# Kernel tuning notes

Hardware: AMD Instinct MI355X
Metric: run time of the kernel (lower is better)

## Reference

```python
import jax, jax.numpy as jnp
import numpy as np
from jax import lax

EPS = 1e-6  # LayerNorm2d eps


def _ln2d(x, w, b):
    # channel-wise LayerNorm over dim 1 of [B,C,H,W]
    mu = jnp.mean(x, axis=1, keepdims=True)
    var = jnp.mean((x - mu) ** 2, axis=1, keepdims=True)
    return (x - mu) / jnp.sqrt(var + EPS) * w[None, :, None, None] + b[None, :, None, None]


def _conv1x1(x, w, b):
    # w: [O, C]
    return jnp.einsum('bchw,oc->bohw', x, w) + b[None, :, None, None]


def _dconv(x, w, b):
    # 3x3 conv, dilation 4, padding 4 -> same H,W. w: [O, C, 3, 3]
    y = lax.conv_general_dilated(x, w, window_strides=(1, 1),
                                 padding=((4, 4), (4, 4)), rhs_dilation=(4, 4),
                                 dimension_numbers=('NCHW', 'OIHW', 'NCHW'))
    return y + b[None, :, None, None]


def _forward(x_l, x_r, nl_w, nl_b, nr_w, nr_b, lp1_w, lp1_b, rp1_w, rp1_b,
             dl_w, dl_b, dr_w, dr_b, lp2_w, lp2_b, rp2_w, rp2_b, beta, gamma):
    c = x_l.shape[1]
    scale = c ** (-0.5)
    N_l = _ln2d(x_l, nl_w, nl_b)
    N_r = _ln2d(x_r, nr_w, nr_b)
    V_l = jnp.transpose(_conv1x1(x_l, lp2_w, lp2_b), (0, 2, 3, 1))   # [B,H,W,C]
    V_r = jnp.transpose(_conv1x1(x_r, rp2_w, rp2_b), (0, 2, 3, 1))
    Q_l = jnp.transpose(_conv1x1(N_l, lp1_w, lp1_b), (0, 2, 3, 1))   # [B,H,W,C]
    Q_r = jnp.transpose(_conv1x1(N_r, rp1_w, rp1_b), (0, 2, 3, 1))
    K_l_T = jnp.transpose(_dconv(N_l, dl_w, dl_b), (0, 2, 1, 3))     # [B,H,C,W]
    K_r_T = jnp.transpose(_dconv(N_r, dr_w, dr_b), (0, 2, 1, 3))
    # per-row cross attention: [B,H,W,W]
    attn_r2l = jnp.einsum('bhwc,bhcv->bhwv', Q_l, K_r_T) * scale
    attn_l2r = jnp.einsum('bhwc,bhcv->bhwv', Q_r, K_l_T) * scale
    F_r2l = jnp.einsum('bhwv,bhvc->bhwc', jax.nn.softmax(attn_r2l, axis=-1), V_r)
    F_l2r = jnp.einsum('bhwv,bhvc->bhwc', jax.nn.softmax(attn_l2r, axis=-1), V_l)
    F_r2l = jnp.transpose(F_r2l, (0, 3, 1, 2)) * beta   # [B,C,H,W]
    F_l2r = jnp.transpose(F_l2r, (0, 3, 1, 2)) * gamma
    return x_l + F_r2l, x_r + F_l2r


def setup_inputs() -> dict:
    key = jax.random.key(0)
    ks = jax.random.split(key, 12)
    B, C, H, W = 2, 128, 192, 512
    s = 0.02
    rn = lambda k, shp: s * jax.random.normal(k, shp, jnp.float32)
    return {
        'x_l': jax.random.normal(ks[0], (B, C, H, W), jnp.float32),
        'x_r': jax.random.normal(ks[1], (B, C, H, W), jnp.float32),
        'nl_w': jnp.ones((C,), jnp.float32), 'nl_b': jnp.zeros((C,), jnp.float32),
        'nr_w': jnp.ones((C,), jnp.float32), 'nr_b': jnp.zeros((C,), jnp.float32),
        'lp1_w': rn(ks[2], (C, C)), 'lp1_b': jnp.zeros((C,), jnp.float32),
        'rp1_w': rn(ks[3], (C, C)), 'rp1_b': jnp.zeros((C,), jnp.float32),
        'dl_w': rn(ks[4], (C, C, 3, 3)), 'dl_b': jnp.zeros((C,), jnp.float32),
        'dr_w': rn(ks[5], (C, C, 3, 3)), 'dr_b': jnp.zeros((C,), jnp.float32),
        'lp2_w': rn(ks[6], (C, C)), 'lp2_b': jnp.zeros((C,), jnp.float32),
        'rp2_w': rn(ks[7], (C, C)), 'rp2_b': jnp.zeros((C,), jnp.float32),
        'beta': 0.1 * jax.random.normal(ks[8], (1, C, 1, 1), jnp.float32),
        'gamma': 0.1 * jax.random.normal(ks[9], (1, C, 1, 1), jnp.float32),
    }


def reference(x_l, x_r, nl_w, nl_b, nr_w, nr_b, lp1_w, lp1_b, rp1_w, rp1_b,
              dl_w, dl_b, dr_w, dr_b, lp2_w, lp2_b, rp2_w, rp2_b, beta, gamma):
    return _forward(x_l, x_r, nl_w, nl_b, nr_w, nr_b, lp1_w, lp1_b, rp1_w, rp1_b,
                    dl_w, dl_b, dr_w, dr_b, lp2_w, lp2_b, rp2_w, rp2_b, beta, gamma)
```

## Files before the change

kernel.cpp:

```cpp
#include <hip/hip_runtime.h>
#include <stdint.h>

#define CC 128
#define HH 192
#define WW 512
#define BB 2
#define HW (HH*WW)
#define CHW (CC*HW)
#define TENS (BB*CHW)

typedef __attribute__((ext_vector_type(8))) short bf16x8;
typedef __attribute__((ext_vector_type(4))) short bf16x4;
typedef __attribute__((ext_vector_type(4))) float f32x4;

__device__ __forceinline__ unsigned short f2bf(float f) {
    union { float f; unsigned u; } v; v.f = f;
    return (unsigned short)((v.u + 0x7FFFu + ((v.u >> 16) & 1u)) >> 16);
}
__device__ __forceinline__ float bf2f(unsigned short u) {
    union { unsigned u; float f; } v; v.u = ((unsigned)u) << 16;
    return v.f;
}
__device__ __forceinline__ uint32_t cvtpk(float lo, float hi) {
    uint32_t r;
    asm("v_cvt_pk_bf16_f32 %0, %1, %2" : "=v"(r) : "v"(lo), "v"(hi));
    return r;
}
__device__ __forceinline__ f32x4 MFMA(bf16x8 a, bf16x8 b, f32x4 c) {
    return __builtin_amdgcn_mfma_f32_16x16x32_bf16(a, b, c, 0, 0, 0);
}
__device__ __forceinline__ f32x4 MFMA16(bf16x4 a, bf16x4 b, f32x4 c) {
#if __has_builtin(__builtin_amdgcn_mfma_f32_16x16x16_bf16)
    return __builtin_amdgcn_mfma_f32_16x16x16_bf16(a, b, c, 0, 0, 0);
#elif __has_builtin(__builtin_amdgcn_mfma_f32_16x16x16bf16_1k)
    return __builtin_amdgcn_mfma_f32_16x16x16bf16_1k(a, b, c, 0, 0, 0);
#else
    f32x4 d = c;
    asm("v_mfma_f32_16x16x16_bf16 %0, %1, %2, %0" : "+v"(d) : "v"(a), "v"(b));
    return d;
#endif
}

__global__ __launch_bounds__(256) void wcast_k(
    const float* __restrict__ dlw, const float* __restrict__ drw,
    unsigned short* __restrict__ wd)
{
    int i = blockIdx.x * 256 + threadIdx.x;
    if (i >= 2 * 9 * CC * CC) return;
    int e  = i & 7;
    int l  = (i >> 3) & 63;
    int n_ = (i >> 9) & 3;
    int kk = (i >> 11) & 3;
    int oh = (i >> 13) & 1;
    int rest = i >> 14;
    int tap = rest % 9;
    int side = rest / 9;
    int o = oh * 64 + n_ * 16 + (l & 15);
    int c = kk * 32 + (l >> 4) * 8 + e;
    const float* src = side ? drw : dlw;
    wd[i] = f2bf(src[((size_t)o * CC + c) * 9 + tap]);
}

__global__ __launch_bounds__(256) void lnv_k(
    const float* __restrict__ xl, const float* __restrict__ xr,
    const float* __restrict__ nlw, const float* __restrict__ nlb,
    const float* __restrict__ nrw, const float* __restrict__ nrb,
    const float* __restrict__ wlp, const float* __restrict__ blp,
    const float* __restrict__ wrp, const float* __restrict__ brp,
    unsigned short* __restrict__ ntl, unsigned short* __restrict__ ntr,
    unsigned short* __restrict__ vlo, unsigned short* __restrict__ vro)
{
    const int side = blockIdx.y;
    const float* x  = side ? xr : xl;
    const float* nw = side ? nrw : nlw;
    const float* nb = side ? nrb : nlb;
    const float* wv = side ? wrp : wlp;
    const float* bv = side ? brp : blp;
    unsigned short* nt = side ? ntr : ntl;
    unsigned short* vo = side ? vro : vlo;
    const int bid = blockIdx.x;
    const int wt = bid & 7, h = (bid >> 3) % HH, b = bid / (8 * HH);
    const int w0 = wt * 64;
    const int t = threadIdx.x;

    __shared__ unsigned short sA[64][136];
    __shared__ unsigned short sB[128][136];
    __shared__ float red[8][64];
    __shared__ float smu[64], srs[64];

    {
        const int w = t & 63, cg = t >> 6;
        const float* xp = x + (size_t)b * CHW + (size_t)h * WW + w0 + w;
        float s = 0.f, q = 0.f;
        for (int i = 0; i < 16; i++) {
            int c = cg * 32 + i * 2;
            float v0 = xp[(size_t)c * HW];
            float v1 = xp[(size_t)(c + 1) * HW];
            *(uint32_t*)&sA[w][c] = cvtpk(v0, v1);
            s += v0 + v1; q += v0 * v0 + v1 * v1;
        }
        red[cg][w] = s; red[4 + cg][w] = q;
    }
    for (int it = 0; it < 16; it++) {
        int f = it * 1024 + t * 4;
        int o = f >> 7, c = f & 127;
        float4 v = *(const float4*)(wv + o * CC + c);
        *(uint32_t*)&sB[o][c]     = cvtpk(v.x, v.y);
        *(uint32_t*)&sB[o][c + 2] = cvtpk(v.z, v.w);
    }
    __syncthreads();
    if (t < 64) {
        float S = red[0][t] + red[1][t] + red[2][t] + red[3][t];
        float Q = red[4][t] + red[5][t] + red[6][t] + red[7][t];
        float mu = S * (1.f / CC);
        float var = fmaxf(Q * (1.f / CC) - mu * mu, 0.f);
        smu[t] = mu; srs[t] = rsqrtf(var + 1e-6f);
    }
    __syncthreads();
    {
        const int cl = (t & 63) * 2, wg = t >> 6;
        const float nwa = nw[cl], nwb = nw[cl + 1];
        const float nba = nb[cl], nbb = nb[cl + 1];
        unsigned short* npb = nt + ((size_t)(b * HH + h) * WW + w0) * CC;
        for (int wp = 0; wp < 16; wp++) {
            int w = wp * 4 + wg;
            float mu = smu[w], rs = srs[w];
            float v0 = (bf2f(sA[w][cl]) - mu) * rs * nwa + nba;
            float v1 = (bf2f(sA[w][cl + 1]) - mu) * rs * nwb + nbb;
            *(uint32_t*)&npb[(size_t)w * CC + cl] = cvtpk(v0, v1);
        }
    }
    const int wid = t >> 6, l = t & 63, lr = l & 15, lg = l >> 4;
    f32x4 acc[8] = {};
    for (int kk = 0; kk < 4; kk++) {
        bf16x8 a = *(const bf16x8*)&sA[wid * 16 + lr][kk * 32 + lg * 8];
#pragma unroll
        for (int n_ = 0; n_ < 8; n_++) {
            bf16x8 bb = *(const bf16x8*)&sB[n_ * 16 + lr][kk * 32 + lg * 8];
            acc[n_] = MFMA(a, bb, acc[n_]);
        }
    }
    unsigned short* vp = vo + ((size_t)(b * HH + h) * CC) * WW + w0;
    for (int n_ = 0; n_ < 8; n_++) {
        int o = n_ * 16 + lr;
        float bias = bv[o];
        uint2 uu;
        uu.x = cvtpk(acc[n_][0] + bias, acc[n_][1] + bias);
        uu.y = cvtpk(acc[n_][2] + bias, acc[n_][3] + bias);
        *(uint2*)&vp[(size_t)o * WW + wid * 16 + lg * 4] = uu;
    }
}

__global__ __launch_bounds__(256) void dconv_k(
    const unsigned short* __restrict__ ntl, const unsigned short* __restrict__ ntr,
    const unsigned short* __restrict__ wfr,
    const float* __restrict__ dlb, const float* __restrict__ drb,
    unsigned short* __restrict__ klo, unsigned short* __restrict__ kro)
{
    const int side = blockIdx.y;
    const unsigned short* nt = side ? ntr : ntl;
    const unsigned short* wbase = wfr + (size_t)side * 9 * 16384;
    const float* bd = side ? drb : dlb;
    unsigned short* ko = side ? kro : klo;
    const int bid0 = blockIdx.x;
    const int lgc = (bid0 & 7) * 192 + (bid0 >> 3);
    const int wt = lgc & 3;
    const int hb = lgc >> 2;
    const int h = hb % HH, b = hb / HH;
    const int w0 = wt * 128;
    const int t = threadIdx.x;
    const int wid = t >> 6, l = t & 63, lr = l & 15, lg = l >> 4;
    const int whalf = wid & 1, ohalf = wid >> 1;

    __shared__ unsigned short sA[136][136];

    f32x4 acc[4][4] = {};
    for (int dy = 0; dy < 3; dy++) {
        const int hh = h + 4 * (dy - 1);
        const bool hok = (hh >= 0 && hh < HH);
        __syncthreads();
        for (int f = t * 8; f < 136 * 128; f += 2048) {
            int wloc = f >> 7, c = f & 127;
            int w = w0 - 4 + wloc;
            bf16x8 v = {0, 0, 0, 0, 0, 0, 0, 0};
            if (hok && w >= 0 && w < WW)
                v = *(const bf16x8*)(nt + ((size_t)(b * HH + hh) * WW + w) * CC + c);
            *(bf16x8*)&sA[wloc][c] = v;
        }
        __syncthreads();
#pragma unroll
        for (int dx = 0; dx < 3; dx++) {
            const unsigned short* wtap =
                wbase + (size_t)(dy * 3 + dx) * 16384 + ohalf * 8192 + l * 8;
#pragma unroll
            for (int kk = 0; kk < 4; kk++) {
                bf16x8 bfr[4];
#pragma unroll
                for (int n_ = 0; n_ < 4; n_++)
                    bfr[n_] = *(const bf16x8*)(wtap + (kk * 4 + n_) * 512);
                bf16x8 af[4];
#pragma unroll
                for (int g = 0; g < 4; g++)
                    af[g] = *(const bf16x8*)&sA[whalf * 64 + g * 16 + lr + 4 * dx][kk * 32 + lg * 8];
#pragma unroll
                for (int g = 0; g < 4; g++)
#pragma unroll
                    for (int n_ = 0; n_ < 4; n_++)
                        acc[g][n_] = MFMA(af[g], bfr[n_], acc[g][n_]);
            }
        }
    }
    unsigned short* kp = ko + ((size_t)(b * HH + h) * WW + w0) * CC;
    for (int g = 0; g < 4; g++)
        for (int n_ = 0; n_ < 4; n_++) {
            int o = ohalf * 64 + n_ * 16 + lr;
            float bias = bd[o];
            for (int j = 0; j < 4; j++) {
                int w = whalf * 64 + g * 16 + lg * 4 + j;
                kp[(size_t)w * CC + o] = f2bf(acc[g][n_][j] + bias);
            }
        }
}

__global__ __launch_bounds__(256, 2) void attn_k(
    const unsigned short* __restrict__ ntl, const unsigned short* __restrict__ ntr,
    const unsigned short* __restrict__ kl,  const unsigned short* __restrict__ kr,
    const unsigned short* __restrict__ vtl, const unsigned short* __restrict__ vtr,
    const float* __restrict__ lp1w, const float* __restrict__ lp1b,
    const float* __restrict__ rp1w, const float* __restrict__ rp1b,
    const float* __restrict__ xl, const float* __restrict__ xr,
    const float* __restrict__ beta, const float* __restrict__ gamma,
    float* __restrict__ out)
{
    __shared__ __align__(16) char smem[52224];
    unsigned short* sQ  = (unsigned short*)smem;
    unsigned short* sWh = (unsigned short*)(smem + 34816);
    unsigned short* sKt = (unsigned short*)smem;
    unsigned short* sVt = (unsigned short*)(smem + 17408);

    const int dir = blockIdx.z;
    const unsigned short* nq  = dir ? ntr : ntl;
    const unsigned short* kws = dir ? kl : kr;
    const unsigned short* vws = dir ? vtl : vtr;
    const float* wq   = dir ? rp1w : lp1w;
    const float* bq   = dir ? rp1b : lp1b;
    const float* xres = dir ? xr : xl;
    const float* mult = dir ? gamma : beta;
    float* op = out + (size_t)dir * TENS;

    const int bid = blockIdx.x;
    const int xcd = bid & 7;
    const int s   = bid >> 3;
    const int qb  = s & 3;
    const int bh  = xcd + 8 * (s >> 2);
    const int q0  = qb * 128;
    const int t = threadIdx.x;
    const int wid = t >> 6, l = t & 63, lr = l & 15, lg = l >> 4;

    const unsigned short* ksrc = kws + (size_t)bh * WW * CC;
    const unsigned short* vsrc = vws + (size_t)bh * CC * WW;

    bf16x8 kreg[4], vreg[4];
#pragma unroll
    for (int it = 0; it < 4; it++) {
        int f = it * 2048 + t * 8;
        kreg[it] = *(const bf16x8*)(ksrc + f);
    }
#pragma unroll
    for (int it = 0; it < 4; it++) {
        int f = it * 2048 + t * 8;
        int c = f >> 6, k = f & 63;
        vreg[it] = *(const bf16x8*)(vsrc + (size_t)c * WW + k);
    }

    {
        const unsigned short* nsrc = nq + ((size_t)bh * WW + q0) * CC;
        for (int it = 0; it < 8; it++) {
            int f = it * 2048 + t * 8;
            *(bf16x8*)&sQ[(f >> 7) * 136 + (f & 127)] = *(const bf16x8*)(nsrc + f);
        }
        for (int it = 0; it < 8; it++) {
            int f = it * 1024 + t * 4;
            int o = f >> 7, c = f & 127;
            float4 v = *(const float4*)(wq + o * CC + c);
            *(uint32_t*)&sWh[o * 136 + c]     = cvtpk(v.x, v.y);
            *(uint32_t*)&sWh[o * 136 + c + 2] = cvtpk(v.z, v.w);
        }
    }
    f32x4 qacc[2][8] = {};
    __syncthreads();
    for (int kk = 0; kk < 4; kk++) {
        bf16x8 a0 = *(const bf16x8*)&sQ[(wid * 32 + lr) * 136 + kk * 32 + lg * 8];
        bf16x8 a1 = *(const bf16x8*)&sQ[(wid * 32 + 16 + lr) * 136 + kk * 32 + lg * 8];
#pragma unroll
        for (int n_ = 0; n_ < 4; n_++) {
            bf16x8 b = *(const bf16x8*)&sWh[(n_ * 16 + lr) * 136 + kk * 32 + lg * 8];
            qacc[0][n_] = MFMA(a0, b, qacc[0][n_]);
            qacc[1][n_] = MFMA(a1, b, qacc[1][n_]);
        }
    }
    __syncthreads();
    for (int it = 0; it < 8; it++) {
        int f = it * 1024 + t * 4;
        int o = f >> 7, c = f & 127;
        float4 v = *(const float4*)(wq + (o + 64) * CC + c);
        *(uint32_t*)&sWh[o * 136 + c]     = cvtpk(v.x, v.y);
        *(uint32_t*)&sWh[o * 136 + c + 2] = cvtpk(v.z, v.w);
    }
    __syncthreads();
    for (int kk = 0; kk < 4; kk++) {
        bf16x8 a0 = *(const bf16x8*)&sQ[(wid * 32 + lr) * 136 + kk * 32 + lg * 8];
        bf16x8 a1 = *(const bf16x8*)&sQ[(wid * 32 + 16 + lr) * 136 + kk * 32 + lg * 8];
#pragma unroll
        for (int n_ = 0; n_ < 4; n_++) {
            bf16x8 b = *(const bf16x8*)&sWh[(n_ * 16 + lr) * 136 + kk * 32 + lg * 8];
            qacc[0][4 + n_] = MFMA(a0, b, qacc[0][4 + n_]);
            qacc[1][4 + n_] = MFMA(a1, b, qacc[1][4 + n_]);
        }
    }
    __syncthreads();
    {
        const float SCL = 0.08838834764831845f * 1.4426950408889634f;
#pragma unroll
        for (int mg = 0; mg < 2; mg++)
#pragma unroll
            for (int n_ = 0; n_ < 8; n_++) {
                float bias = bq[n_ * 16 + lr];
#pragma unroll
                for (int j = 0; j < 4; j++)
                    sQ[(wid * 32 + mg * 16 + lg * 4 + j) * 136 + n_ * 16 + lr] =
                        f2bf((qacc[mg][n_][j] + bias) * SCL);
            }
    }
    __syncthreads();
    bf16x8 qf[2][4];
#pragma unroll
    for (int qg = 0; qg < 2; qg++)
#pragma unroll
        for (int kk = 0; kk < 4; kk++)
            qf[qg][kk] = *(const bf16x8*)&sQ[(wid * 32 + qg * 16 + lr) * 136 + kk * 32 + lg * 8];

    f32x4 oacc[8][2] = {};
    float mrow[2] = {-1e30f, -1e30f};
    float lrow[2] = {0.f, 0.f};

    for (int kb = 0; kb < 8; kb++) {
        __syncthreads();
#pragma unroll
        for (int it = 0; it < 4; it++) {
            int f = it * 2048 + t * 8;
            *(bf16x8*)&sKt[(f >> 7) * 136 + (f & 127)] = kreg[it];
        }
#pragma unroll
        for (int it = 0; it < 4; it++) {
            int f = it * 2048 + t * 8;
            int c = f >> 6, k = f & 63;
            *(bf16x8*)&sVt[c * 72 + k] = vreg[it];
        }
        if (kb < 7) {
#pragma unroll
            for (int it = 0; it < 4; it++) {
                int f = it * 2048 + t * 8;
                kreg[it] = *(const bf16x8*)(ksrc + (kb + 1) * 64 * CC + f);
            }
#pragma unroll
            for (int it = 0; it < 4; it++) {
                int f = it * 2048 + t * 8;
                int c = f >> 6, k = f & 63;
                vreg[it] = *(const bf16x8*)(vsrc + (size_t)c * WW + (kb + 1) * 64 + k);
            }
        }
        __syncthreads();
        f32x4 sacc[2][4] = {};
        __builtin_amdgcn_s_setprio(1);
        for (int kk = 0; kk < 4; kk++)
#pragma unroll
            for (int n_ = 0; n_ < 4; n_++) {
                bf16x8 kf = *(const bf16x8*)&sKt[(n_ * 16 + lr) * 136 + kk * 32 + lg * 8];
                sacc[0][n_] = MFMA(kf, qf[0][kk], sacc[0][n_]);
                sacc[1][n_] = MFMA(kf, qf[1][kk], sacc[1][n_]);
            }
        __builtin_amdgcn_s_setprio(0);
        float pm[2];
#pragma unroll
        for (int qg = 0; qg < 2; qg++) {
            float m_ = sacc[qg][0][0];
#pragma unroll
            for (int n_ = 0; n_ < 4; n_++)
#pragma unroll
                for (int j = 0; j < 4; j++) m_ = fmaxf(m_, sacc[qg][n_][j]);
            m_ = fmaxf(m_, __shfl_xor(m_, 16, 64));
            m_ = fmaxf(m_, __shfl_xor(m_, 32, 64));
            pm[qg] = m_;
        }
        bool need = (pm[0] - mrow[0] > 8.f) || (pm[1] - mrow[1] > 8.f);
        if (__any(need)) {
            float al[2];
#pragma unroll
            for (int qg = 0; qg < 2; qg++) {
                float mn = fmaxf(mrow[qg], pm[qg]);
                al[qg] = exp2f(mrow[qg] - mn);
                mrow[qg] = mn;
                lrow[qg] *= al[qg];
            }
#pragma unroll
            for (int n_ = 0; n_ < 8; n_++)
#pragma unroll
                for (int qg = 0; qg < 2; qg++) {
                    f32x4 o = oacc[n_][qg];
                    o[0] *= al[qg]; o[1] *= al[qg]; o[2] *= al[qg]; o[3] *= al[qg];
                    oacc[n_][qg] = o;
                }
        }
#pragma unroll
        for (int qg = 0; qg < 2; qg++) {
            float rs = 0.f;
#pragma unroll
            for (int n_ = 0; n_ < 4; n_++)
#pragma unroll
                for (int j = 0; j < 4; j++) {
                    float e = exp2f(sacc[qg][n_][j] - mrow[qg]);
                    sacc[qg][n_][j] = e;
                    rs += e;
                }
            rs += __shfl_xor(rs, 16, 64);
            rs += __shfl_xor(rs, 32, 64);
            lrow[qg] += rs;
        }
        __builtin_amdgcn_s_setprio(1);
#pragma unroll
        for (int n_ = 0; n_ < 4; n_++) {
            union { uint32_t u[2]; bf16x4 v; } b0, b1;
            b0.u[0] = cvtpk(sacc[0][n_][0], sacc[0][n_][1]);
            b0.u[1] = cvtpk(sacc[0][n_][2], sacc[0][n_][3]);
            b1.u[0] = cvtpk(sacc[1][n_][0], sacc[1][n_][1]);
            b1.u[1] = cvtpk(sacc[1][n_][2], sacc[1][n_][3]);
#pragma unroll
            for (int n8 = 0; n8 < 8; n8++) {
                bf16x4 va = *(const bf16x4*)&sVt[(n8 * 16 + lr) * 72 + n_ * 16 + lg * 4];
                oacc[n8][0] = MFMA16(va, b0.v, oacc[n8][0]);
                oacc[n8][1] = MFMA16(va, b1.v, oacc[n8][1]);
            }
        }
        __builtin_amdgcn_s_setprio(0);
    }

    const float inv0 = 1.f / lrow[0], inv1 = 1.f / lrow[1];
    const int b = bh / HH, h = bh % HH;
    const int w_0 = q0 + wid * 32 + lr;
    const float* xp0 = xres + (size_t)b * CHW + (size_t)h * WW + w_0;
    float* outp0 = op + (size_t)b * CHW + (size_t)h * WW + w_0;
#pragma unroll
    for (int n_ = 0; n_ < 8; n_++) {
        float4 m4 = *(const float4*)&mult[n_ * 16 + lg * 4];
#pragma unroll
        for (int j = 0; j < 4; j++) {
            int c = n_ * 16 + lg * 4 + j;
            float mj = (&m4.x)[j];
            outp0[(size_t)c * HW]      = xp0[(size_t)c * HW]      + oacc[n_][0][j] * inv0 * mj;
            outp0[(size_t)c * HW + 16] = xp0[(size_t)c * HW + 16] + oacc[n_][1][j] * inv1 * mj;
        }
    }
}

extern "C" void kernel_launch(void* const* d_in, const int* in_sizes, int n_in,
                              void* d_out, int out_size, void* d_ws, size_t ws_size,
                              hipStream_t stream)
{
    const float* xl   = (const float*)d_in[0];
    const float* xr   = (const float*)d_in[1];
    const float* nlw  = (const float*)d_in[2];
    const float* nlb  = (const float*)d_in[3];
    const float* nrw  = (const float*)d_in[4];
    const float* nrb  = (const float*)d_in[5];
    const float* lp1w = (const float*)d_in[6];
    const float* lp1b = (const float*)d_in[7];
    const float* rp1w = (const float*)d_in[8];
    const float* rp1b = (const float*)d_in[9];
    const float* dlw  = (const float*)d_in[10];
    const float* dlb  = (const float*)d_in[11];
    const float* drw  = (const float*)d_in[12];
    const float* drb  = (const float*)d_in[13];
    const float* lp2w = (const float*)d_in[14];
    const float* lp2b = (const float*)d_in[15];
    const float* rp2w = (const float*)d_in[16];
    const float* rp2b = (const float*)d_in[17];
    const float* beta = (const float*)d_in[18];
    const float* gamma= (const float*)d_in[19];
    float* out = (float*)d_out;

    unsigned short* ws = (unsigned short*)d_ws;
    const size_t A = (size_t)TENS;
    unsigned short* Ntl = ws;
    unsigned short* Ntr = ws + A;
    unsigned short* Kl  = ws + 2 * A;
    unsigned short* Kr  = ws + 3 * A;
    unsigned short* Vtl = ws + 4 * A;
    unsigned short* Vtr = ws + 5 * A;
    unsigned short* Wd  = ws + 6 * A;

    wcast_k<<<dim3(1152), 256, 0, stream>>>(dlw, drw, Wd);
    lnv_k<<<dim3(3072, 2), 256, 0, stream>>>(xl, xr, nlw, nlb, nrw, nrb,
        lp2w, lp2b, rp2w, rp2b, Ntl, Ntr, Vtl, Vtr);
    dconv_k<<<dim3(1536, 2), 256, 0, stream>>>(Ntl, Ntr, Wd, dlb, drb, Kl, Kr);
    attn_k<<<dim3(1536, 1, 2), 256, 0, stream>>>(Ntl, Ntr, Kl, Kr, Vtl, Vtr,
        lp1w, lp1b, rp1w, rp1b, xl, xr, beta, gamma, out);
}
```

Before: 505.7 us.

## Load K/V tiles directly to LDS with XOR swizzle, raise occupancy

Replaces the register-staged prefetch of K and V tiles with direct global-to-LDS loads, using an XOR-swizzled layout instead of padded rows to avoid bank conflicts. This frees the staging registers, and the launch bound is raised so three blocks can share a CU. Without the register double-buffering, the load for each tile is no longer overlapped with the previous tile's compute, so stalls at the barrier may grow.

```diff
diff --git a/kernel.cpp b/kernel.cpp
--- a/kernel.cpp
+++ b/kernel.cpp
@@ -39,6 +39,11 @@
     asm("v_mfma_f32_16x16x16_bf16 %0, %1, %2, %0" : "+v"(d) : "v"(a), "v"(b));
     return d;
 #endif
+}
+__device__ __forceinline__ void gload_lds16(const void* g, void* l) {
+    __builtin_amdgcn_global_load_lds(
+        (const __attribute__((address_space(1))) void*)g,
+        (__attribute__((address_space(3))) void*)l, 16, 0, 0);
 }
 
 __global__ __launch_bounds__(256) void wcast_k(
@@ -222,7 +227,7 @@
         }
 }
 
-__global__ __launch_bounds__(256, 2) void attn_k(
+__global__ __launch_bounds__(256, 3) void attn_k(
     const unsigned short* __restrict__ ntl, const unsigned short* __restrict__ ntr,
     const unsigned short* __restrict__ kl,  const unsigned short* __restrict__ kr,
     const unsigned short* __restrict__ vtl, const unsigned short* __restrict__ vtr,
@@ -235,8 +240,6 @@
     __shared__ __align__(16) char smem[52224];
     unsigned short* sQ  = (unsigned short*)smem;
     unsigned short* sWh = (unsigned short*)(smem + 34816);
-    unsigned short* sKt = (unsigned short*)smem;
-    unsigned short* sVt = (unsigned short*)(smem + 17408);
 
     const int dir = blockIdx.z;
     const unsigned short* nq  = dir ? ntr : ntl;
@@ -260,17 +263,18 @@
     const unsigned short* ksrc = kws + (size_t)bh * WW * CC;
     const unsigned short* vsrc = vws + (size_t)bh * CC * WW;
 
-    bf16x8 kreg[4], vreg[4];
+    int koff[4], voff[4];
 #pragma unroll
     for (int it = 0; it < 4; it++) {
-        int f = it * 2048 + t * 8;
-        kreg[it] = *(const bf16x8*)(ksrc + f);
+        int row = it * 16 + wid * 4 + (l >> 4);
+        int gci = (l & 15) ^ (row & 7);
+        koff[it] = row * CC + gci * 8;
     }
 #pragma unroll
     for (int it = 0; it < 4; it++) {
-        int f = it * 2048 + t * 8;
-        int c = f >> 6, k = f & 63;
-        vreg[it] = *(const bf16x8*)(vsrc + (size_t)c * WW + k);
+        int row = it * 32 + wid * 8 + (l >> 3);
+        int gci = (l & 7) ^ (row & 7);
+        voff[it] = row * WW + gci * 8;
     }
 
     {
@@ -343,32 +347,19 @@
     f32x4 oacc[8][2] = {};
     float mrow[2] = {-1e30f, -1e30f};
     float lrow[2] = {0.f, 0.f};
+    const int lr7 = lr & 7;
 
     for (int kb = 0; kb < 8; kb++) {
         __syncthreads();
-#pragma unroll
-        for (int it = 0; it < 4; it++) {
-            int f = it * 2048 + t * 8;
-            *(bf16x8*)&sKt[(f >> 7) * 136 + (f & 127)] = kreg[it];
-        }
-#pragma unroll
-        for (int it = 0; it < 4; it++) {
-            int f = it * 2048 + t * 8;
-            int c = f >> 6, k = f & 63;
-            *(bf16x8*)&sVt[c * 72 + k] = vreg[it];
-        }
-        if (kb < 7) {
-#pragma unroll
-            for (int it = 0; it < 4; it++) {
-                int f = it * 2048 + t * 8;
-                kreg[it] = *(const bf16x8*)(ksrc + (kb + 1) * 64 * CC + f);
-            }
-#pragma unroll
-            for (int it = 0; it < 4; it++) {
-                int f = it * 2048 + t * 8;
-                int c = f >> 6, k = f & 63;
-                vreg[it] = *(const bf16x8*)(vsrc + (size_t)c * WW + (kb + 1) * 64 + k);
-            }
+        {
+            const unsigned short* kS = ksrc + kb * 64 * CC;
+            const unsigned short* vS = vsrc + kb * 64;
+#pragma unroll
+            for (int it = 0; it < 4; it++)
+                gload_lds16(kS + koff[it], smem + it * 4096 + wid * 1024);
+#pragma unroll
+            for (int it = 0; it < 4; it++)
+                gload_lds16(vS + voff[it], smem + 16384 + it * 4096 + wid * 1024);
         }
         __syncthreads();
         f32x4 sacc[2][4] = {};
@@ -376,7 +367,8 @@
         for (int kk = 0; kk < 4; kk++)
 #pragma unroll
             for (int n_ = 0; n_ < 4; n_++) {
-                bf16x8 kf = *(const bf16x8*)&sKt[(n_ * 16 + lr) * 136 + kk * 32 + lg * 8];
+                bf16x8 kf = *(const bf16x8*)(smem + (n_ * 16 + lr) * 256
+                                             + (((kk * 4 + lg) ^ lr7) << 4));
                 sacc[0][n_] = MFMA(kf, qf[0][kk], sacc[0][n_]);
                 sacc[1][n_] = MFMA(kf, qf[1][kk], sacc[1][n_]);
             }
@@ -437,7 +429,9 @@
             b1.u[1] = cvtpk(sacc[1][n_][2], sacc[1][n_][3]);
 #pragma unroll
             for (int n8 = 0; n8 < 8; n8++) {
-                bf16x4 va = *(const bf16x4*)&sVt[(n8 * 16 + lr) * 72 + n_ * 16 + lg * 4];
+                bf16x4 va = *(const bf16x4*)(smem + 16384 + (n8 * 16 + lr) * 128
+                                             + ((((n_ * 2) + (lg >> 1)) ^ lr7) << 4)
+                                             + ((lg & 1) << 3));
                 oacc[n8][0] = MFMA16(va, b0.v, oacc[n8][0]);
                 oacc[n8][1] = MFMA16(va, b1.v, oacc[n8][1]);
             }
```

Measured after the change: 523.3 us. 3.5% more time.
